# Kernel optimization log

Measured on AMD Instinct MI355X. Metric: run time of the kernel, lower is better.

Reference implementation:

```python
import jax, jax.numpy as jnp
import numpy as np
from jax import lax

T, B, E, H, L = 256, 128, 512, 1024, 2


def setup_inputs() -> dict:
    key = jax.random.key(0)
    ks = jax.random.split(key, 12)
    x = jax.random.normal(ks[0], (T, B, E), dtype=jnp.float32)
    # PackedSequence batch_sizes: descending, first == max batch
    bs = jnp.sort(jax.random.randint(ks[1], (T,), 1, B + 1).astype(jnp.int32))[::-1]
    bs = bs.at[0].set(B)
    unsorted_indices = jax.random.permutation(ks[2], B).astype(jnp.int32)
    s = 1.0 / np.sqrt(H)
    def u(k, shape):
        return jax.random.uniform(k, shape, jnp.float32, -s, s)
    return {
        "x": x,
        "W_ih0": u(ks[3], (3 * H, E)), "W_hh0": u(ks[4], (3 * H, H)),
        "b_ih0": u(ks[5], (3 * H,)), "b_hh0": u(ks[6], (3 * H,)),
        "W_ih1": u(ks[7], (3 * H, H)), "W_hh1": u(ks[8], (3 * H, H)),
        "b_ih1": u(ks[9], (3 * H,)), "b_hh1": u(ks[10], (3 * H,)),
        "batch_sizes": bs,
        "unsorted_indices": unsorted_indices,
    }


def gru_cell(x, h, W_ih, W_hh, b_ih, b_hh):
    gi = x @ W_ih.T + b_ih          # [b, 3H]
    gh = h @ W_hh.T + b_hh          # [b, 3H]
    i_r, i_z, i_n = jnp.split(gi, 3, axis=-1)
    h_r, h_z, h_n = jnp.split(gh, 3, axis=-1)
    r = jax.nn.sigmoid(i_r + h_r)
    z = jax.nn.sigmoid(i_z + h_z)
    n = jnp.tanh(i_n + r * h_n)
    return (1.0 - z) * n + z * h


def reference(x, W_ih0, W_hh0, b_ih0, b_hh0, W_ih1, W_hh1, b_ih1, b_hh1,
              batch_sizes, unsorted_indices):
    params = [(W_ih0, W_hh0, b_ih0, b_hh0), (W_ih1, W_hh1, b_ih1, b_hh1)]
    row = jnp.arange(B)

    def step(h, inp):
        xt, bs = inp                       # xt: [B, E]
        mask = (row < bs)[:, None]         # active rows this timestep
        layer_in = xt
        new_h = []
        for i in range(L):
            hn = gru_cell(layer_in, h[i], *params[i])
            # inactive rows keep their previous hidden state (packed-seq semantics)
            new_h.append(jnp.where(mask, hn, h[i]))
            layer_in = hn
        return jnp.stack(new_h), None

    h0 = jnp.zeros((L, B, H), dtype=x.dtype)
    h_final, _ = lax.scan(step, h0, (x, batch_sizes))
    # index_select(h, 1, unsorted_indices)
    return h_final[:, unsorted_indices, :]
```

## Files before the change

kernel.cpp:

```cpp
#include <hip/hip_runtime.h>
#include <cstdint>
#include <cstddef>

#define T_ 256
#define B_ 128
#define E_ 512
#define H_ 1024
#define BH (B_*H_)
#define GI (B_*3072)

typedef _Float16 v8h __attribute__((ext_vector_type(8)));
typedef float    v4f __attribute__((ext_vector_type(4)));
typedef unsigned int u32x4 __attribute__((ext_vector_type(4)));

__device__ __forceinline__ float sigmoidf_(float x) {
    return 1.0f / (1.0f + __expf(-x));
}
__device__ __forceinline__ float tanhf_(float x) {
    return 1.0f - 2.0f / (__expf(2.0f * x) + 1.0f);
}

__device__ __forceinline__ void sc_store2(void* p, unsigned v) {
    asm volatile("global_store_short %0, %1, off sc0 sc1" :: "v"(p), "v"(v) : "memory");
}
__device__ __forceinline__ void sc_store4(void* p, float v) {
    asm volatile("global_store_dword %0, %1, off sc0 sc1" :: "v"(p), "v"(v) : "memory");
}

__global__ __launch_bounds__(256, 1) void gru_persist(
    const int* __restrict__ bs,
    const _Float16* __restrict__ x16,
    const _Float16* __restrict__ Wi0,
    const _Float16* __restrict__ Wh0,
    const _Float16* __restrict__ Wi1,
    const _Float16* __restrict__ Wh1,
    const float* __restrict__ bias,
    float* __restrict__ h0f, float* __restrict__ h1f,
    _Float16* __restrict__ h0h, _Float16* __restrict__ h1h,
    _Float16* __restrict__ hn0,
    float* __restrict__ gi0, float* __restrict__ gi1,
    int* __restrict__ barctr)
{
    __shared__ _Float16 WL[16 * 48 * 72];
    __shared__ _Float16 AS[2][128][72];

    const int bid = blockIdx.x;
    const int grp = bid >> 6;
    const int sl  = bid & 63;
    const int tid = threadIdx.x;
    const int lane = tid & 63, w = tid >> 6;
    const int m = lane & 15, q = lane >> 4;

    {
        const _Float16* Wsrc; int K;
        if      (grp == 0) { Wsrc = Wi0; K = 512;  }
        else if (grp == 1) { Wsrc = Wh0; K = 1024; }
        else if (grp == 2) { Wsrc = Wi1; K = 1024; }
        else               { Wsrc = Wh1; K = 1024; }
        const bool isAB = (grp & 1);
        const int nchw = K / 64;
        for (int u = tid; u < nchw * 384; u += 256) {
            int kc = u / 384, rem = u % 384, c = rem >> 3, slot = rem & 7;
            int gr = isAB ? ((c >> 4) * 1024 + sl * 16 + (c & 15)) : (sl * 48 + c);
            *(u32x4*)&WL[(kc * 48 + c) * 72 + slot * 8] =
                *(const u32x4*)(Wsrc + (size_t)gr * K + kc * 64 + slot * 8);
        }
    }
    __syncthreads();

    const int colG = sl * 16 + m;
    float br = 0.f, bz = 0.f, bi = 0.f, bh = 0.f;
    if (grp & 1) {
        const float* bb = bias + (grp == 3 ? 4 * H_ : 0);
        br = bb[colG]; bz = bb[H_ + colG];
        bi = bb[2 * H_ + colG]; bh = bb[3 * H_ + colG];
    }

    float hm[2][4];
#pragma unroll
    for (int rf = 0; rf < 2; ++rf)
#pragma unroll
        for (int r = 0; r < 4; ++r) hm[rf][r] = 0.f;

    const int srow = tid >> 1, spart = tid & 1;

    int* shard  = barctr + (bid & 7) * 256;
    int* master = barctr + 8 * 256;
    int* epoch  = barctr + 9 * 256;

    v4f acc[6];
    u32x4 QA0, QA1, QA2, QA3, QB0, QB1, QB2, QB3;
    u32x4 QC0, QC1, QC2, QC3, QD0, QD1, QD2, QD3;

#define ISSUE(Qv, kcn) do { \
        const _Float16* p_ = sp + (size_t)(kcn) * 64; \
        Qv##0 = *(const u32x4*)(p_ + 0);  Qv##1 = *(const u32x4*)(p_ + 8); \
        Qv##2 = *(const u32x4*)(p_ + 16); Qv##3 = *(const u32x4*)(p_ + 24); \
    } while (0)
#define WRITEQ(Qv, dbuf) do { \
        _Float16* d_ = &AS[dbuf][srow][spart * 32]; \
        *(u32x4*)(d_ + 0) = Qv##0;  *(u32x4*)(d_ + 8)  = Qv##1; \
        *(u32x4*)(d_ + 16) = Qv##2; *(u32x4*)(d_ + 24) = Qv##3; \
    } while (0)
#define COMPUTE(BUF, KC) do { \
        const _Float16* wch_ = &WL[(KC) * 48 * 72]; \
        _Pragma("unroll") \
        for (int s = 0; s < 2; ++s) { \
            const int ko = s * 32 + q * 8; \
            v8h a0 = *(const v8h*)&AS[BUF][32 * w + m][ko]; \
            v8h a1 = *(const v8h*)&AS[BUF][32 * w + 16 + m][ko]; \
            _Pragma("unroll") \
            for (int g = 0; g < 3; ++g) { \
                v8h b = *(const v8h*)&wch_[(g * 16 + m) * 72 + ko]; \
                acc[g * 2 + 0] = __builtin_amdgcn_mfma_f32_16x16x32_f16(a0, b, acc[g * 2 + 0], 0, 0, 0); \
                acc[g * 2 + 1] = __builtin_amdgcn_mfma_f32_16x16x32_f16(a1, b, acc[g * 2 + 1], 0, 0, 0); \
            } \
        } \
    } while (0)
#define CHUNK_BODY(KC, QI, QW, BUF) do { \
        if ((KC) + 4 < nch) ISSUE(QI, (KC) + 4); \
        COMPUTE(BUF, KC); \
        if ((KC) + 1 < nch) WRITEQ(QW, (BUF) ^ 1); \
        __syncthreads(); \
    } while (0)

    for (int k = 0; k < T_ + 3; ++k) {
        const int t = (grp == 0) ? k : (grp == 1) ? k - 1 : (grp == 2) ? k - 2 : k - 3;
        const bool active = (t >= 0) && (t < T_);

        if (active) {
            const int pb = t & 1;
            const int rb = pb ^ 1;
            const _Float16* Abase; int ap, nch;
            if      (grp == 0) { Abase = x16 + (size_t)t * B_ * E_;  ap = E_; nch = 8;  }
            else if (grp == 1) { Abase = h0h + (size_t)rb * BH;      ap = H_; nch = 16; }
            else if (grp == 2) { Abase = hn0 + (size_t)pb * BH;      ap = H_; nch = 16; }
            else               { Abase = h1h + (size_t)rb * BH;      ap = H_; nch = 16; }

#pragma unroll
            for (int i = 0; i < 6; ++i) acc[i] = (v4f){0.f, 0.f, 0.f, 0.f};

            const _Float16* sp = Abase + (size_t)srow * ap + spart * 32;

            ISSUE(QA, 0); ISSUE(QB, 1); ISSUE(QC, 2); ISSUE(QD, 3);
            WRITEQ(QA, 0);
            __syncthreads();

            for (int base = 0; base < nch; base += 4) {
                CHUNK_BODY(base + 0, QA, QB, 0);
                CHUNK_BODY(base + 1, QB, QC, 1);
                CHUNK_BODY(base + 2, QC, QD, 0);
                CHUNK_BODY(base + 3, QD, QA, 1);
            }

            if (grp == 0 || grp == 2) {
                float* gw = (grp == 0 ? gi0 : gi1) + (size_t)pb * GI;
                const int cbase = sl * 48;
#pragma unroll
                for (int cf = 0; cf < 3; ++cf)
#pragma unroll
                    for (int rf = 0; rf < 2; ++rf)
#pragma unroll
                        for (int r = 0; r < 4; ++r) {
                            int row = 32 * w + rf * 16 + q * 4 + r;
                            sc_store4(gw + (size_t)row * 3072 + cbase + cf * 16 + m,
                                      acc[cf * 2 + rf][r]);
                        }
            } else {
                const int bs_t = bs[t];
                const float* gr_ = (grp == 1 ? gi0 : gi1) + (size_t)pb * GI;
                _Float16*   hh_w = (grp == 1 ? h0h : h1h) + (size_t)pb * BH;
                _Float16*   hn0w = hn0 + (size_t)pb * BH;
#pragma unroll
                for (int rf = 0; rf < 2; ++rf)
#pragma unroll
                    for (int r = 0; r < 4; ++r) {
                        int row = 32 * w + rf * 16 + q * 4 + r;
                        size_t go = (size_t)row * 3072 + colG;
                        float gir = gr_[go];
                        float giz = gr_[go + 1024];
                        float gin = gr_[go + 2048];
                        size_t off = (size_t)row * H_ + colG;
                        float hprev = hm[rf][r];
                        float rr = sigmoidf_(gir + acc[0 + rf][r] + br);
                        float zz = sigmoidf_(giz + acc[2 + rf][r] + bz);
                        float nn = tanhf_(gin + bi + rr * (acc[4 + rf][r] + bh));
                        float hnew = (1.0f - zz) * nn + zz * hprev;
                        bool act = row < bs_t;
                        float hsel = act ? hnew : hprev;
                        if (grp == 1)
                            sc_store2(hn0w + off, (unsigned)__builtin_bit_cast(unsigned short, (_Float16)hnew));
                        sc_store2(hh_w + off, (unsigned)__builtin_bit_cast(unsigned short, (_Float16)hsel));
                        hm[rf][r] = hsel;
                    }
            }
        }

        if (k < T_ + 2) {
            __syncthreads();
            if (tid == 0) {
                int old = __hip_atomic_fetch_add(shard, 1, __ATOMIC_RELAXED, __HIP_MEMORY_SCOPE_AGENT);
                if (old + 1 == 32 * (k + 1)) {
                    int mo = __hip_atomic_fetch_add(master, 1, __ATOMIC_RELAXED, __HIP_MEMORY_SCOPE_AGENT);
                    if (mo + 1 == 8 * (k + 1))
                        __hip_atomic_store(epoch, k + 1, __ATOMIC_RELEASE, __HIP_MEMORY_SCOPE_AGENT);
                }
                while (__hip_atomic_load(epoch, __ATOMIC_RELAXED, __HIP_MEMORY_SCOPE_AGENT) < k + 1)
                    __builtin_amdgcn_s_sleep(2);
                (void)__hip_atomic_load(epoch, __ATOMIC_ACQUIRE, __HIP_MEMORY_SCOPE_AGENT);
            }
            __syncthreads();
        }
    }

    if (grp & 1) {
        float* hf = (grp == 1) ? h0f : h1f;
#pragma unroll
        for (int rf = 0; rf < 2; ++rf)
#pragma unroll
            for (int r = 0; r < 4; ++r) {
                int row = 32 * w + rf * 16 + q * 4 + r;
                hf[(size_t)row * H_ + colG] = hm[rf][r];
            }
    }
#undef ISSUE
#undef WRITEQ
#undef COMPUTE
#undef CHUNK_BODY
}

__global__ void cvt_f32_f16(const float* __restrict__ s, _Float16* __restrict__ d, int n) {
    int i = (blockIdx.x * 256 + threadIdx.x) * 8;
    if (i >= n) return;
    float4 v0 = *(const float4*)(s + i);
    float4 v1 = *(const float4*)(s + i + 4);
    v8h o = { (_Float16)v0.x, (_Float16)v0.y, (_Float16)v0.z, (_Float16)v0.w,
              (_Float16)v1.x, (_Float16)v1.y, (_Float16)v1.z, (_Float16)v1.w };
    *(v8h*)(d + i) = o;
}

__global__ void prep_bias(const float* __restrict__ bi0, const float* __restrict__ bh0,
                          const float* __restrict__ bi1, const float* __restrict__ bh1,
                          float* __restrict__ bias) {
    int tid = blockIdx.x * 256 + threadIdx.x;
    int l = tid >> 10, j = tid & 1023;
    const float* bi = l ? bi1 : bi0;
    const float* bh = l ? bh1 : bh0;
    float* o = bias + l * 4 * H_;
    o[j]           = bi[j] + bh[j];
    o[H_ + j]      = bi[H_ + j] + bh[H_ + j];
    o[2 * H_ + j]  = bi[2 * H_ + j];
    o[3 * H_ + j]  = bh[2 * H_ + j];
}

__global__ void gather_out(const float* __restrict__ h0f, const float* __restrict__ h1f,
                           const int* __restrict__ unsorted, float* __restrict__ out) {
    int rowid = blockIdx.x;
    int l = rowid >> 7, b = rowid & 127;
    int src = unsorted[b];
    const float* s = (l ? h1f : h0f) + (size_t)src * H_;
    float* o = out + (size_t)rowid * H_;
    int c = threadIdx.x * 4;
    *(float4*)(o + c) = *(const float4*)(s + c);
}

extern "C" void kernel_launch(void* const* d_in, const int* in_sizes, int n_in,
                              void* d_out, int out_size, void* d_ws, size_t ws_size,
                              hipStream_t stream) {
    const float* x    = (const float*)d_in[0];
    const float* Wi0f = (const float*)d_in[1];
    const float* Wh0f = (const float*)d_in[2];
    const float* bi0  = (const float*)d_in[3];
    const float* bh0  = (const float*)d_in[4];
    const float* Wi1f = (const float*)d_in[5];
    const float* Wh1f = (const float*)d_in[6];
    const float* bi1  = (const float*)d_in[7];
    const float* bh1  = (const float*)d_in[8];
    const int*  bs       = (const int*)d_in[9];
    const int*  unsorted = (const int*)d_in[10];
    float* out = (float*)d_out;

    char* ws = (char*)d_ws;
    size_t off = 0;
    auto alloc = [&](size_t bytes) -> char* {
        char* p = ws + off;
        off += (bytes + 255) & ~(size_t)255;
        return p;
    };
    _Float16* x16 = (_Float16*)alloc((size_t)T_ * B_ * E_ * 2);
    _Float16* Wi0 = (_Float16*)alloc((size_t)3 * H_ * E_ * 2);
    _Float16* Wh0 = (_Float16*)alloc((size_t)3 * H_ * H_ * 2);
    _Float16* Wi1 = (_Float16*)alloc((size_t)3 * H_ * H_ * 2);
    _Float16* Wh1 = (_Float16*)alloc((size_t)3 * H_ * H_ * 2);
    float*    bias = (float*)alloc(2 * 4 * H_ * 4);
    float*    gi0  = (float*)alloc((size_t)2 * GI * 4);
    float*    gi1  = (float*)alloc((size_t)2 * GI * 4);
    float*    h0f  = (float*)alloc((size_t)BH * 4);
    float*    h1f  = (float*)alloc((size_t)BH * 4);
    char* zbase = ws + off;
    _Float16* h0h = (_Float16*)alloc((size_t)2 * BH * 2);
    _Float16* h1h = (_Float16*)alloc((size_t)2 * BH * 2);
    _Float16* hn0 = (_Float16*)alloc((size_t)2 * BH * 2);
    int*      barctr = (int*)alloc(16 * 1024);
    size_t zbytes = (size_t)((ws + off) - zbase);

    (void)hipMemsetAsync(zbase, 0, zbytes, stream);

    cvt_f32_f16<<<(T_ * B_ * E_) / 2048, 256, 0, stream>>>(x, x16, T_ * B_ * E_);
    cvt_f32_f16<<<(3 * H_ * E_) / 2048, 256, 0, stream>>>(Wi0f, Wi0, 3 * H_ * E_);
    cvt_f32_f16<<<(3 * H_ * H_) / 2048, 256, 0, stream>>>(Wh0f, Wh0, 3 * H_ * H_);
    cvt_f32_f16<<<(3 * H_ * H_) / 2048, 256, 0, stream>>>(Wi1f, Wi1, 3 * H_ * H_);
    cvt_f32_f16<<<(3 * H_ * H_) / 2048, 256, 0, stream>>>(Wh1f, Wh1, 3 * H_ * H_);
    prep_bias<<<8, 256, 0, stream>>>(bi0, bh0, bi1, bh1, bias);

    gru_persist<<<256, 256, 0, stream>>>(bs, x16, Wi0, Wh0, Wi1, Wh1, bias,
                                         h0f, h1f, h0h, h1h, hn0, gi0, gi1, barctr);
    gather_out<<<256, 256, 0, stream>>>(h0f, h1f, unsorted, out);
}
```

Baseline: 4.855 ms.

## Fuse layer-1 input and hidden GEMMs per block and use flag-based grid barrier

```diff
diff --git a/kernel.cpp b/kernel.cpp
--- a/kernel.cpp
+++ b/kernel.cpp
@@ -8,6 +8,7 @@
 #define H_ 1024
 #define BH (B_*H_)
 #define GI (B_*3072)
+#define GATHER_BID 64
 
 typedef _Float16 v8h __attribute__((ext_vector_type(8)));
 typedef float    v4f __attribute__((ext_vector_type(4)));
@@ -38,55 +39,63 @@
     float* __restrict__ h0f, float* __restrict__ h1f,
     _Float16* __restrict__ h0h, _Float16* __restrict__ h1h,
     _Float16* __restrict__ hn0,
-    float* __restrict__ gi0, float* __restrict__ gi1,
-    int* __restrict__ barctr)
+    float* __restrict__ gi0,
+    int* __restrict__ flags,
+    int* __restrict__ epoch)
 {
-    __shared__ _Float16 WL[16 * 48 * 72];
+    __shared__ _Float16 WL[55296];
     __shared__ _Float16 AS[2][128][72];
 
     const int bid = blockIdx.x;
-    const int grp = bid >> 6;
-    const int sl  = bid & 63;
     const int tid = threadIdx.x;
     const int lane = tid & 63, w = tid >> 6;
     const int m = lane & 15, q = lane >> 4;
-
-    {
-        const _Float16* Wsrc; int K;
-        if      (grp == 0) { Wsrc = Wi0; K = 512;  }
-        else if (grp == 1) { Wsrc = Wh0; K = 1024; }
-        else if (grp == 2) { Wsrc = Wi1; K = 1024; }
-        else               { Wsrc = Wh1; K = 1024; }
-        const bool isAB = (grp & 1);
-        const int nchw = K / 64;
-        for (int u = tid; u < nchw * 384; u += 256) {
+    const int srow = tid >> 1, spart = tid & 1;
+    const int stage = (bid < 64) ? 0 : (bid < 128) ? 1 : 2;
+    const int sl = (stage == 0) ? bid : (stage == 1) ? bid - 64 : bid - 128;
+
+    if (stage == 0) {
+        for (int u = tid; u < 8 * 384; u += 256) {
             int kc = u / 384, rem = u % 384, c = rem >> 3, slot = rem & 7;
-            int gr = isAB ? ((c >> 4) * 1024 + sl * 16 + (c & 15)) : (sl * 48 + c);
+            int gr = sl * 48 + c;
             *(u32x4*)&WL[(kc * 48 + c) * 72 + slot * 8] =
-                *(const u32x4*)(Wsrc + (size_t)gr * K + kc * 64 + slot * 8);
+                *(const u32x4*)(Wi0 + (size_t)gr * E_ + kc * 64 + slot * 8);
+        }
+    } else if (stage == 1) {
+        for (int u = tid; u < 16 * 384; u += 256) {
+            int kc = u / 384, rem = u % 384, c = rem >> 3, slot = rem & 7;
+            int gr = (c >> 4) * 1024 + sl * 16 + (c & 15);
+            *(u32x4*)&WL[(kc * 48 + c) * 72 + slot * 8] =
+                *(const u32x4*)(Wh0 + (size_t)gr * H_ + kc * 64 + slot * 8);
+        }
+    } else {
+        for (int u = tid; u < 32 * 192; u += 256) {
+            int kc = u / 192, rem = u % 192, c = rem >> 3, slot = rem & 7;
+            int gr = (c >> 3) * 1024 + sl * 8 + (c & 7);
+            const _Float16* src = (kc < 16) ? (Wi1 + (size_t)gr * H_ + kc * 64)
+                                            : (Wh1 + (size_t)gr * H_ + (kc - 16) * 64);
+            *(u32x4*)&WL[(kc * 24 + c) * 72 + slot * 8] = *(const u32x4*)(src + slot * 8);
         }
     }
     __syncthreads();
 
-    const int colG = sl * 16 + m;
     float br = 0.f, bz = 0.f, bi = 0.f, bh = 0.f;
-    if (grp & 1) {
-        const float* bb = bias + (grp == 3 ? 4 * H_ : 0);
-        br = bb[colG]; bz = bb[H_ + colG];
-        bi = bb[2 * H_ + colG]; bh = bb[3 * H_ + colG];
+    int colE = 0;
+    if (stage == 1) {
+        colE = sl * 16 + m;
+        br = bias[colE]; bz = bias[H_ + colE];
+        bi = bias[2 * H_ + colE]; bh = bias[3 * H_ + colE];
+    } else if (stage == 2) {
+        colE = sl * 8 + (m & 7);
+        const float* bb = bias + 4 * H_;
+        br = bb[colE]; bz = bb[H_ + colE];
+        bi = bb[2 * H_ + colE]; bh = bb[3 * H_ + colE];
     }
-
     float hm[2][4];
 #pragma unroll
     for (int rf = 0; rf < 2; ++rf)
 #pragma unroll
         for (int r = 0; r < 4; ++r) hm[rf][r] = 0.f;
-
-    const int srow = tid >> 1, spart = tid & 1;
-
-    int* shard  = barctr + (bid & 7) * 256;
-    int* master = barctr + 8 * 256;
-    int* epoch  = barctr + 9 * 256;
 
     v4f acc[6];
     u32x4 QA0, QA1, QA2, QA3, QB0, QB1, QB2, QB3;
@@ -102,7 +111,7 @@
         *(u32x4*)(d_ + 0) = Qv##0;  *(u32x4*)(d_ + 8)  = Qv##1; \
         *(u32x4*)(d_ + 16) = Qv##2; *(u32x4*)(d_ + 24) = Qv##3; \
     } while (0)
-#define COMPUTE(BUF, KC) do { \
+#define COMPUTE3(BUF, KC) do { \
         const _Float16* wch_ = &WL[(KC) * 48 * 72]; \
         _Pragma("unroll") \
         for (int s = 0; s < 2; ++s) { \
@@ -117,44 +126,101 @@
             } \
         } \
     } while (0)
-#define CHUNK_BODY(KC, QI, QW, BUF) do { \
+#define CHUNK3(KC, QI, QW, BUF) do { \
         if ((KC) + 4 < nch) ISSUE(QI, (KC) + 4); \
-        COMPUTE(BUF, KC); \
+        COMPUTE3(BUF, KC); \
         if ((KC) + 1 < nch) WRITEQ(QW, (BUF) ^ 1); \
         __syncthreads(); \
     } while (0)
-
-    for (int k = 0; k < T_ + 3; ++k) {
-        const int t = (grp == 0) ? k : (grp == 1) ? k - 1 : (grp == 2) ? k - 2 : k - 3;
-        const bool active = (t >= 0) && (t < T_);
-
-        if (active) {
-            const int pb = t & 1;
-            const int rb = pb ^ 1;
-            const _Float16* Abase; int ap, nch;
-            if      (grp == 0) { Abase = x16 + (size_t)t * B_ * E_;  ap = E_; nch = 8;  }
-            else if (grp == 1) { Abase = h0h + (size_t)rb * BH;      ap = H_; nch = 16; }
-            else if (grp == 2) { Abase = hn0 + (size_t)pb * BH;      ap = H_; nch = 16; }
-            else               { Abase = h1h + (size_t)rb * BH;      ap = H_; nch = 16; }
-
-#pragma unroll
-            for (int i = 0; i < 6; ++i) acc[i] = (v4f){0.f, 0.f, 0.f, 0.f};
-
-            const _Float16* sp = Abase + (size_t)srow * ap + spart * 32;
-
-            ISSUE(QA, 0); ISSUE(QB, 1); ISSUE(QC, 2); ISSUE(QD, 3);
-            WRITEQ(QA, 0);
-            __syncthreads();
-
-            for (int base = 0; base < nch; base += 4) {
-                CHUNK_BODY(base + 0, QA, QB, 0);
-                CHUNK_BODY(base + 1, QB, QC, 1);
-                CHUNK_BODY(base + 2, QC, QD, 0);
-                CHUNK_BODY(base + 3, QD, QA, 1);
-            }
-
-            if (grp == 0 || grp == 2) {
-                float* gw = (grp == 0 ? gi0 : gi1) + (size_t)pb * GI;
+#define COMPUTE2(BUF, KC, ANB) do { \
+        const _Float16* wch_ = &WL[(KC) * 24 * 72]; \
+        _Pragma("unroll") \
+        for (int s = 0; s < 2; ++s) { \
+            const int ko = s * 32 + q * 8; \
+            v8h a0 = *(const v8h*)&AS[BUF][32 * w + m][ko]; \
+            v8h a1 = *(const v8h*)&AS[BUF][32 * w + 16 + m][ko]; \
+            v8h b0 = *(const v8h*)&wch_[(m) * 72 + ko]; \
+            v8h b1 = *(const v8h*)&wch_[(8 + m) * 72 + ko]; \
+            acc[0] = __builtin_amdgcn_mfma_f32_16x16x32_f16(a0, b0, acc[0], 0, 0, 0); \
+            acc[1] = __builtin_amdgcn_mfma_f32_16x16x32_f16(a1, b0, acc[1], 0, 0, 0); \
+            acc[(ANB) + 0] = __builtin_amdgcn_mfma_f32_16x16x32_f16(a0, b1, acc[(ANB) + 0], 0, 0, 0); \
+            acc[(ANB) + 1] = __builtin_amdgcn_mfma_f32_16x16x32_f16(a1, b1, acc[(ANB) + 1], 0, 0, 0); \
+        } \
+    } while (0)
+#define CHUNK2(KC, QI, QW, BUF, KB, ANB) do { \
+        if ((KC) + 4 < 16) ISSUE(QI, (KC) + 4); \
+        COMPUTE2((KC) + (KB), BUF, ANB); \
+    } while (0)
+#define SUBLOOP2(KB, ANB) do { \
+        ISSUE(QA, 0); ISSUE(QB, 1); ISSUE(QC, 2); ISSUE(QD, 3); \
+        WRITEQ(QA, 0); \
+        __syncthreads(); \
+        for (int base = 0; base < 16; base += 4) { \
+            if (base + 4 < 16) ISSUE(QA, base + 4); \
+            COMPUTE2(0, (KB) + base + 0, ANB); \
+            if (base + 1 < 16) WRITEQ(QB, 1); \
+            __syncthreads(); \
+            if (base + 5 < 16) ISSUE(QB, base + 5); \
+            COMPUTE2(1, (KB) + base + 1, ANB); \
+            if (base + 2 < 16) WRITEQ(QC, 0); \
+            __syncthreads(); \
+            if (base + 6 < 16) ISSUE(QC, base + 6); \
+            COMPUTE2(0, (KB) + base + 2, ANB); \
+            if (base + 3 < 16) WRITEQ(QD, 1); \
+            __syncthreads(); \
+            if (base + 7 < 16) ISSUE(QD, base + 7); \
+            COMPUTE2(1, (KB) + base + 3, ANB); \
+            if (base + 4 < 16) WRITEQ(QA, 0); \
+            __syncthreads(); \
+        } \
+    } while (0)
+
+#define WAIT_EPOCH(KV, DO_INV) do { \
+        if (tid == 0) { \
+            while (__hip_atomic_load(epoch, __ATOMIC_RELAXED, __HIP_MEMORY_SCOPE_AGENT) < (KV)) \
+                __builtin_amdgcn_s_sleep(1); \
+            if (DO_INV) (void)__hip_atomic_load(epoch, __ATOMIC_ACQUIRE, __HIP_MEMORY_SCOPE_AGENT); \
+        } \
+        __syncthreads(); \
+    } while (0)
+#define DO_BARRIER(KV) do { \
+        __syncthreads(); \
+        if (tid == 0) \
+            __hip_atomic_store(&flags[bid], (KV) + 1, __ATOMIC_RELEASE, __HIP_MEMORY_SCOPE_AGENT); \
+        if (bid == GATHER_BID && tid < 64) { \
+            const int tgt = (KV) + 1; \
+            for (;;) { \
+                int f0 = __hip_atomic_load(&flags[tid],       __ATOMIC_RELAXED, __HIP_MEMORY_SCOPE_AGENT); \
+                int f1 = __hip_atomic_load(&flags[tid + 64],  __ATOMIC_RELAXED, __HIP_MEMORY_SCOPE_AGENT); \
+                int f2 = __hip_atomic_load(&flags[tid + 128], __ATOMIC_RELAXED, __HIP_MEMORY_SCOPE_AGENT); \
+                int f3 = __hip_atomic_load(&flags[tid + 192], __ATOMIC_RELAXED, __HIP_MEMORY_SCOPE_AGENT); \
+                bool ok = (f0 >= tgt) && (f1 >= tgt) && (f2 >= tgt) && (f3 >= tgt); \
+                if (__all(ok)) break; \
+                __builtin_amdgcn_s_sleep(1); \
+            } \
+            if (tid == 0) \
+                __hip_atomic_store(epoch, (KV) + 1, __ATOMIC_RELEASE, __HIP_MEMORY_SCOPE_AGENT); \
+        } \
+    } while (0)
+
+    for (int k = 0; k < T_ + 2; ++k) {
+        if (stage == 0) {
+            const bool active = (k < T_);
+            if (active) {
+                const int t = k;
+#pragma unroll
+                for (int i = 0; i < 6; ++i) acc[i] = (v4f){0.f, 0.f, 0.f, 0.f};
+                const _Float16* sp = x16 + (size_t)t * B_ * E_ + (size_t)srow * E_ + spart * 32;
+                const int nch = 8;
+                ISSUE(QA, 0); ISSUE(QB, 1); ISSUE(QC, 2); ISSUE(QD, 3);
+                WRITEQ(QA, 0);
+                __syncthreads();
+                CHUNK3(0, QA, QB, 0); CHUNK3(1, QB, QC, 1);
+                CHUNK3(2, QC, QD, 0); CHUNK3(3, QD, QA, 1);
+                CHUNK3(4, QA, QB, 0); CHUNK3(5, QB, QC, 1);
+                CHUNK3(6, QC, QD, 0); CHUNK3(7, QD, QA, 1);
+                WAIT_EPOCH(k, false);
+                float* gw = gi0 + (size_t)(t & 1) * GI;
                 const int cbase = sl * 48;
 #pragma unroll
                 for (int cf = 0; cf < 3; ++cf)
@@ -166,21 +232,38 @@
                             sc_store4(gw + (size_t)row * 3072 + cbase + cf * 16 + m,
                                       acc[cf * 2 + rf][r]);
                         }
-            } else {
+            }
+        } else if (stage == 1) {
+            const bool active = (k >= 1) && (k <= T_);
+            if (active) {
+                const int t = k - 1;
+                WAIT_EPOCH(k, true);
                 const int bs_t = bs[t];
-                const float* gr_ = (grp == 1 ? gi0 : gi1) + (size_t)pb * GI;
-                _Float16*   hh_w = (grp == 1 ? h0h : h1h) + (size_t)pb * BH;
-                _Float16*   hn0w = hn0 + (size_t)pb * BH;
+                const int pb = t & 1, rb = pb ^ 1;
+#pragma unroll
+                for (int i = 0; i < 6; ++i) acc[i] = (v4f){0.f, 0.f, 0.f, 0.f};
+                const _Float16* sp = h0h + (size_t)rb * BH + (size_t)srow * H_ + spart * 32;
+                const int nch = 16;
+                ISSUE(QA, 0); ISSUE(QB, 1); ISSUE(QC, 2); ISSUE(QD, 3);
+                WRITEQ(QA, 0);
+                __syncthreads();
+                for (int base = 0; base < 16; base += 4) {
+                    CHUNK3(base + 0, QA, QB, 0); CHUNK3(base + 1, QB, QC, 1);
+                    CHUNK3(base + 2, QC, QD, 0); CHUNK3(base + 3, QD, QA, 1);
+                }
+                const float* gr_ = gi0 + (size_t)pb * GI;
+                _Float16* hh_w = h0h + (size_t)pb * BH;
+                _Float16* hn0w = hn0 + (size_t)pb * BH;
 #pragma unroll
                 for (int rf = 0; rf < 2; ++rf)
 #pragma unroll
                     for (int r = 0; r < 4; ++r) {
                         int row = 32 * w + rf * 16 + q * 4 + r;
-                        size_t go = (size_t)row * 3072 + colG;
+                        size_t go = (size_t)row * 3072 + colE;
                         float gir = gr_[go];
                         float giz = gr_[go + 1024];
                         float gin = gr_[go + 2048];
-                        size_t off = (size_t)row * H_ + colG;
+                        size_t off = (size_t)row * H_ + colE;
                         float hprev = hm[rf][r];
                         float rr = sigmoidf_(gir + acc[0 + rf][r] + br);
                         float zz = sigmoidf_(giz + acc[2 + rf][r] + bz);
@@ -188,45 +271,75 @@
                         float hnew = (1.0f - zz) * nn + zz * hprev;
                         bool act = row < bs_t;
                         float hsel = act ? hnew : hprev;
-                        if (grp == 1)
-                            sc_store2(hn0w + off, (unsigned)__builtin_bit_cast(unsigned short, (_Float16)hnew));
+                        sc_store2(hn0w + off, (unsigned)__builtin_bit_cast(unsigned short, (_Float16)hnew));
                         sc_store2(hh_w + off, (unsigned)__builtin_bit_cast(unsigned short, (_Float16)hsel));
+                        hm[rf][r] = hsel;
+                    }
+            } else if (bid == GATHER_BID) {
+                WAIT_EPOCH(k, false);
+            }
+        } else {
+            const bool active = (k >= 2);
+            if (active) {
+                const int t = k - 2;
+                WAIT_EPOCH(k, true);
+                const int bs_t = bs[t];
+                const int pb = t & 1, rb = pb ^ 1;
+#pragma unroll
+                for (int i = 0; i < 6; ++i) acc[i] = (v4f){0.f, 0.f, 0.f, 0.f};
+                {
+                    const _Float16* sp = hn0 + (size_t)pb * BH + (size_t)srow * H_ + spart * 32;
+                    SUBLOOP2(0, 2);
+                }
+                {
+                    const _Float16* sp = h1h + (size_t)rb * BH + (size_t)srow * H_ + spart * 32;
+                    SUBLOOP2(16, 4);
+                }
+                _Float16* hh_w = h1h + (size_t)pb * BH;
+#pragma unroll
+                for (int rf = 0; rf < 2; ++rf)
+#pragma unroll
+                    for (int r = 0; r < 4; ++r) {
+                        int row = 32 * w + rf * 16 + q * 4 + r;
+                        float zz_s = __shfl_xor(acc[0 + rf][r], 8);
+                        float inx  = __shfl_xor(acc[2 + rf][r], 8);
+                        float hnh  = __shfl_xor(acc[4 + rf][r], 8);
+                        float hprev = hm[rf][r];
+                        float rr = sigmoidf_(acc[0 + rf][r] + br);
+                        float zz = sigmoidf_(zz_s + bz);
+                        float nn = tanhf_(inx + bi + rr * (hnh + bh));
+                        float hnew = (1.0f - zz) * nn + zz * hprev;
+                        bool act = row < bs_t;
+                        float hsel = act ? hnew : hprev;
+                        if (m < 8) {
+                            size_t off = (size_t)row * H_ + colE;
+                            sc_store2(hh_w + off, (unsigned)__builtin_bit_cast(unsigned short, (_Float16)hsel));
+                        }
                         hm[rf][r] = hsel;
                     }
             }
         }
 
-        if (k < T_ + 2) {
-            __syncthreads();
-            if (tid == 0) {
-                int old = __hip_atomic_fetch_add(shard, 1, __ATOMIC_RELAXED, __HIP_MEMORY_SCOPE_AGENT);
-                if (old + 1 == 32 * (k + 1)) {
-                    int mo = __hip_atomic_fetch_add(master, 1, __ATOMIC_RELAXED, __HIP_MEMORY_SCOPE_AGENT);
-                    if (mo + 1 == 8 * (k + 1))
-                        __hip_atomic_store(epoch, k + 1, __ATOMIC_RELEASE, __HIP_MEMORY_SCOPE_AGENT);
-                }
-                while (__hip_atomic_load(epoch, __ATOMIC_RELAXED, __HIP_MEMORY_SCOPE_AGENT) < k + 1)
-                    __builtin_amdgcn_s_sleep(2);
-                (void)__hip_atomic_load(epoch, __ATOMIC_ACQUIRE, __HIP_MEMORY_SCOPE_AGENT);
-            }
-            __syncthreads();
-        }
+        if (k < T_ + 1) DO_BARRIER(k);
     }
 
-    if (grp & 1) {
-        float* hf = (grp == 1) ? h0f : h1f;
+    if (stage == 1) {
 #pragma unroll
         for (int rf = 0; rf < 2; ++rf)
 #pragma unroll
             for (int r = 0; r < 4; ++r) {
                 int row = 32 * w + rf * 16 + q * 4 + r;
-                hf[(size_t)row * H_ + colG] = hm[rf][r];
+                h0f[(size_t)row * H_ + colE] = hm[rf][r];
+            }
+    } else if (stage == 2 && m < 8) {
+#pragma unroll
+        for (int rf = 0; rf < 2; ++rf)
+#pragma unroll
+            for (int r = 0; r < 4; ++r) {
+                int row = 32 * w + rf * 16 + q * 4 + r;
+                h1f[(size_t)row * H_ + colE] = hm[rf][r];
             }
     }
-#undef ISSUE
-#undef WRITEQ
-#undef COMPUTE
-#undef CHUNK_BODY
 }
 
 __global__ void cvt_f32_f16(const float* __restrict__ s, _Float16* __restrict__ d, int n) {
@@ -294,14 +407,14 @@
     _Float16* Wh1 = (_Float16*)alloc((size_t)3 * H_ * H_ * 2);
     float*    bias = (float*)alloc(2 * 4 * H_ * 4);
     float*    gi0  = (float*)alloc((size_t)2 * GI * 4);
-    float*    gi1  = (float*)alloc((size_t)2 * GI * 4);
     float*    h0f  = (float*)alloc((size_t)BH * 4);
     float*    h1f  = (float*)alloc((size_t)BH * 4);
     char* zbase = ws + off;
     _Float16* h0h = (_Float16*)alloc((size_t)2 * BH * 2);
     _Float16* h1h = (_Float16*)alloc((size_t)2 * BH * 2);
     _Float16* hn0 = (_Float16*)alloc((size_t)2 * BH * 2);
-    int*      barctr = (int*)alloc(16 * 1024);
+    int*      flags = (int*)alloc(1024);
+    int*      epoch = (int*)alloc(256);
     size_t zbytes = (size_t)((ws + off) - zbase);
 
     (void)hipMemsetAsync(zbase, 0, zbytes, stream);
@@ -314,6 +427,6 @@
     prep_bias<<<8, 256, 0, stream>>>(bi0, bh0, bi1, bh1, bias);
 
     gru_persist<<<256, 256, 0, stream>>>(bs, x16, Wi0, Wh0, Wi1, Wh1, bias,
-                                         h0f, h1f, h0h, h1h, hn0, gi0, gi1, barctr);
+                                         h0f, h1f, h0h, h1h, hn0, gi0, flags, epoch);
     gather_out<<<256, 256, 0, stream>>>(h0f, h1f, unsorted, out);
 }
```

Result: no change. 4.794 ms (-1.3%).
